# Kernel tuning notes

Measured on AMD Instinct MI355X. Metric: run time of the kernel, lower is better.

## Reference

```python
import jax, jax.numpy as jnp
import numpy as np

NS_STEPS = 10
NS_A, NS_B, NS_C = 3.4445, -4.7750, 2.0315  # standard quintic Newton-Schulz coefficients
EPS = 1e-7

def orthogonalize(w):
    """Newton-Schulz iteration producing a (near-)orthogonal matrix from w."""
    din, dout = w.shape
    transpose = din > dout  # iterate on the wide orientation so X @ X.T is small
    x = w.T if transpose else w
    x = x / (jnp.linalg.norm(x) + EPS)  # spectral norm <= frobenius norm -> contraction

    def body(x, _):
        a = x @ x.T                      # (m, m) Gram matrix
        bmat = NS_B * a + NS_C * (a @ a)
        x = NS_A * x + bmat @ x
        return x, None

    x, _ = jax.lax.scan(body, x, None, length=NS_STEPS)
    return x.T if transpose else x


def setup_inputs() -> dict:
    key = jax.random.key(0)
    k1, k2, k3 = jax.random.split(key, 3)
    B, DIN, DOUT = 16384, 2048, 2048
    x = jax.random.normal(k1, (B, DIN), dtype=jnp.float32)
    w = jax.random.normal(k2, (DIN, DOUT), dtype=jnp.float32)
    b = jax.random.normal(k3, (DOUT,), dtype=jnp.float32) * 0.02
    return {"x": x, "w": w, "b": b}


def reference(x, w, b):
    w_orth = orthogonalize(w)
    return x @ w_orth + b
```

## Files before the change

### kernel.cpp

```cpp
#include <hip/hip_runtime.h>
#include <stdint.h>

typedef unsigned short u16;
typedef _Float16 half_t;
typedef __attribute__((ext_vector_type(4))) float f32x4;
typedef __attribute__((ext_vector_type(8))) _Float16 f16x8;

#define NS_A 3.4445f
#define NS_B -4.7750f
#define NS_C 2.0315f

#define SX      64.0f
#define INV_SX  (1.0f / 64.0f)
#define INV_SA  (1.0f / 4096.0f)

typedef const __attribute__((address_space(1))) void* as1_cvp;
typedef __attribute__((address_space(3))) void* as3_vp;
#define GLOAD_LDS16(gp, lp) \
    __builtin_amdgcn_global_load_lds((as1_cvp)(const void*)(gp), (as3_vp)(void*)(lp), 16, 0, 0)

template <int N> __device__ __forceinline__ void vmwait() {
    if constexpr (N == 0)      asm volatile("s_waitcnt vmcnt(0)" ::: "memory");
    else if constexpr (N == 4) asm volatile("s_waitcnt vmcnt(4)" ::: "memory");
    else if constexpr (N == 6) asm volatile("s_waitcnt vmcnt(6)" ::: "memory");
    else if constexpr (N == 8) asm volatile("s_waitcnt vmcnt(8)" ::: "memory");
    else static_assert(N == 0, "unsupported vmcnt");
}

template <int MODE>
__global__ __launch_bounds__(256, 2) void gemm_ns(
    const half_t* __restrict__ A, const half_t* __restrict__ B,
    const half_t* __restrict__ aux,
    void* __restrict__ outp, half_t* __restrict__ outpT,
    int M, int N, int K)
{
    __shared__ half_t As[3][64 * 64];
    __shared__ half_t Bs[3][128 * 64];
    const int tid  = threadIdx.x;
    const int wid  = tid >> 6;
    const int lane = tid & 63;
    const int wr = wid >> 1, wc = wid & 1;

    int bid = blockIdx.x;
    const int cpx = gridDim.x >> 3;
    bid = (bid & 7) * cpx + (bid >> 3);
    const int nbx  = N / 128;
    const int brow = (bid / nbx) * 64;
    const int bcol = (bid % nbx) * 128;

    f32x4 acc[2][4] = {};

    const int r0   = tid >> 3;
    const int csrc = ((tid & 7) ^ ((tid >> 3) & 7)) * 8;
    const half_t* gA = A + (size_t)(brow + r0) * K + csrc;
    const half_t* gB = B + (size_t)(bcol + r0) * K + csrc;

    auto stage = [&](int slot, int kt) {
#pragma unroll
        for (int j = 0; j < 2; ++j)
            GLOAD_LDS16(gA + (size_t)(j * 32) * K + kt, &As[slot][(j * 256 + wid * 64) * 8]);
#pragma unroll
        for (int j = 0; j < 4; ++j)
            GLOAD_LDS16(gB + (size_t)(j * 32) * K + kt, &Bs[slot][(j * 256 + wid * 64) * 8]);
    };

    f16x8 af[2][2], bf[4][2];
    auto reads = [&](int slot) {
#pragma unroll
        for (int m = 0; m < 2; ++m) {
            const int row = wr * 32 + m * 16 + (lane & 15);
#pragma unroll
            for (int kk = 0; kk < 2; ++kk) {
                const int cc = (kk * 4 + (lane >> 4)) ^ (row & 7);
                af[m][kk] = *(const f16x8*)&As[slot][row * 64 + cc * 8];
            }
        }
#pragma unroll
        for (int n = 0; n < 4; ++n) {
            const int row = wc * 64 + n * 16 + (lane & 15);
#pragma unroll
            for (int kk = 0; kk < 2; ++kk) {
                const int cc = (kk * 4 + (lane >> 4)) ^ (row & 7);
                bf[n][kk] = *(const f16x8*)&Bs[slot][row * 64 + cc * 8];
            }
        }
    };
    auto mfma = [&]() {
        __builtin_amdgcn_s_setprio(1);
#pragma unroll
        for (int kk = 0; kk < 2; ++kk)
#pragma unroll
            for (int m = 0; m < 2; ++m)
#pragma unroll
                for (int n = 0; n < 4; ++n)
                    acc[m][n] = __builtin_amdgcn_mfma_f32_16x16x32_f16(af[m][kk], bf[n][kk], acc[m][n], 0, 0, 0);
        __builtin_amdgcn_s_setprio(0);
    };

    const int nsteps = K / 64;
    stage(0, 0);
    stage(1, 64);
    vmwait<6>();
    __builtin_amdgcn_s_barrier();

    int s = 0;
    for (; s < nsteps - 2; ++s) {
        reads(s % 3);
        stage((s + 2) % 3, (s + 2) * 64);
        vmwait<6>();
        __builtin_amdgcn_s_barrier();
        mfma();
        __builtin_amdgcn_s_barrier();
    }
    reads(s % 3);
    vmwait<0>();
    __builtin_amdgcn_s_barrier();
    mfma();
    __builtin_amdgcn_s_barrier();
    ++s;
    reads(s % 3);
    mfma();

#pragma unroll
    for (int m = 0; m < 2; ++m) {
#pragma unroll
        for (int n = 0; n < 4; ++n) {
            const int row0 = brow + wr * 32 + m * 16 + (lane >> 4) * 4;
            const int col  = bcol + wc * 64 + n * 16 + (lane & 15);
#pragma unroll
            for (int r = 0; r < 4; ++r) {
                const size_t idx = (size_t)(row0 + r) * N + col;
                const float v = acc[m][n][r];
                if (MODE == 0) {
                    ((half_t*)outp)[idx] = (half_t)v;
                } else if (MODE == 1) {
                    ((half_t*)outp)[idx] = (half_t)(NS_B * (float)aux[idx] + NS_C * v * INV_SA);
                } else {
                    const half_t o = (half_t)(NS_A * (float)aux[idx] + v * INV_SA);
                    ((half_t*)outp)[idx] = o;
                    if (outpT) outpT[(size_t)col * M + row0 + r] = o;
                }
            }
        }
    }
}

__global__ __launch_bounds__(512, 2) void gemm_fin(
    const half_t* __restrict__ A, const half_t* __restrict__ B,
    const float* __restrict__ bias, float* __restrict__ out,
    int M, int N, int K)
{
    __shared__ half_t As[4][256 * 32];
    __shared__ half_t Bs[4][256 * 32];
    const int tid  = threadIdx.x;
    const int wid  = tid >> 6;
    const int lane = tid & 63;
    const int wm = wid >> 2;
    const int wn = wid & 3;

    int bid = blockIdx.x;
    const int cpx = gridDim.x >> 3;
    bid = (bid & 7) * cpx + (bid >> 3);
    const int nbx  = N >> 8;
    const int brow = (bid / nbx) << 8;
    const int bcol = (bid % nbx) << 8;

    f32x4 acc[8][4] = {};

    const int r0   = tid >> 2;
    const int csrc = ((tid & 3) ^ ((tid >> 3) & 3)) * 8;
    const half_t* gA = A + (size_t)(brow + r0) * K + csrc;
    const half_t* gB = B + (size_t)(bcol + r0) * K + csrc;

    auto stage = [&](int slot, int kt) {
#pragma unroll
        for (int j = 0; j < 2; ++j)
            GLOAD_LDS16(gA + (size_t)(j * 128) * K + kt, &As[slot][(j * 512 + wid * 64) * 8]);
#pragma unroll
        for (int j = 0; j < 2; ++j)
            GLOAD_LDS16(gB + (size_t)(j * 128) * K + kt, &Bs[slot][(j * 512 + wid * 64) * 8]);
    };

    f16x8 bf[4], af[4];
    auto reads_pre = [&](int slot) {
#pragma unroll
        for (int fc = 0; fc < 4; ++fc) {
            const int row = wn * 64 + fc * 16 + (lane & 15);
            bf[fc] = *(const f16x8*)&Bs[slot][row * 32 + (((lane >> 4) ^ ((row >> 1) & 3)) * 8)];
        }
#pragma unroll
        for (int fr = 0; fr < 4; ++fr) {
            const int row = wm * 128 + fr * 16 + (lane & 15);
            af[fr] = *(const f16x8*)&As[slot][row * 32 + (((lane >> 4) ^ ((row >> 1) & 3)) * 8)];
        }
    };
    auto mfma_all = [&](int slot) {
        __builtin_amdgcn_s_setprio(1);
#pragma unroll
        for (int fr = 0; fr < 4; ++fr)
#pragma unroll
            for (int fc = 0; fc < 4; ++fc)
                acc[fr][fc] = __builtin_amdgcn_mfma_f32_16x16x32_f16(af[fr], bf[fc], acc[fr][fc], 0, 0, 0);
#pragma unroll
        for (int fr = 0; fr < 4; ++fr) {
            const int row = wm * 128 + (fr + 4) * 16 + (lane & 15);
            af[fr] = *(const f16x8*)&As[slot][row * 32 + (((lane >> 4) ^ ((row >> 1) & 3)) * 8)];
        }
#pragma unroll
        for (int fr = 0; fr < 4; ++fr)
#pragma unroll
            for (int fc = 0; fc < 4; ++fc)
                acc[fr + 4][fc] = __builtin_amdgcn_mfma_f32_16x16x32_f16(af[fr], bf[fc], acc[fr + 4][fc], 0, 0, 0);
        __builtin_amdgcn_s_setprio(0);
    };

    const int nsteps = K >> 5;
    stage(0, 0);
    stage(1, 32);
    stage(2, 64);
    vmwait<8>();
    __builtin_amdgcn_s_barrier();

    int s = 0;
    for (; s < nsteps - 3; ++s) {
        reads_pre(s & 3);
        stage((s + 3) & 3, (s + 3) * 32);
        vmwait<8>();
        __builtin_amdgcn_s_barrier();
        mfma_all(s & 3);
        __builtin_amdgcn_s_barrier();
    }
    reads_pre(s & 3);
    vmwait<4>();
    __builtin_amdgcn_s_barrier();
    mfma_all(s & 3);
    __builtin_amdgcn_s_barrier();
    ++s;
    reads_pre(s & 3);
    vmwait<0>();
    __builtin_amdgcn_s_barrier();
    mfma_all(s & 3);
    __builtin_amdgcn_s_barrier();
    ++s;
    reads_pre(s & 3);
    mfma_all(s & 3);

#pragma unroll
    for (int fr = 0; fr < 8; ++fr) {
#pragma unroll
        for (int fc = 0; fc < 4; ++fc) {
            const int row0 = brow + wm * 128 + fr * 16 + (lane >> 4) * 4;
            const int col  = bcol + wn * 64 + fc * 16 + (lane & 15);
            const float bv = bias[col];
#pragma unroll
            for (int r = 0; r < 4; ++r)
                out[(size_t)(row0 + r) * N + col] = acc[fr][fc][r] * INV_SX + bv;
        }
    }
}

__global__ __launch_bounds__(256) void k_sumsq(const float* __restrict__ w,
                                               float* __restrict__ part, int n) {
    __shared__ float s[256];
    const int per  = n / 1024;
    const int base = blockIdx.x * per;
    float acc = 0.f;
    for (int i = threadIdx.x; i < per; i += 256) {
        float v = w[base + i];
        acc += v * v;
    }
    s[threadIdx.x] = acc;
    __syncthreads();
    for (int k = 128; k > 0; k >>= 1) {
        if (threadIdx.x < k) s[threadIdx.x] += s[threadIdx.x + k];
        __syncthreads();
    }
    if (threadIdx.x == 0) part[blockIdx.x] = s[0];
}

__global__ __launch_bounds__(256) void k_scalefin(const float* __restrict__ part,
                                                  float* __restrict__ scale) {
    __shared__ float s[256];
    float acc = 0.f;
    for (int i = threadIdx.x; i < 1024; i += 256) acc += part[i];
    s[threadIdx.x] = acc;
    __syncthreads();
    for (int k = 128; k > 0; k >>= 1) {
        if (threadIdx.x < k) s[threadIdx.x] += s[threadIdx.x + k];
        __syncthreads();
    }
    if (threadIdx.x == 0) scale[0] = SX / (sqrtf(s[0]) + 1e-7f);
}

__global__ __launch_bounds__(256) void k_scale_f16(const float* __restrict__ w,
                                                   const float* __restrict__ scale,
                                                   half_t* __restrict__ o, int n) {
    const int i = (blockIdx.x * 256 + threadIdx.x) * 4;
    if (i < n) {
        const float sc = scale[0];
        float4 v = *(const float4*)(w + i);
        o[i + 0] = (half_t)(v.x * sc);
        o[i + 1] = (half_t)(v.y * sc);
        o[i + 2] = (half_t)(v.z * sc);
        o[i + 3] = (half_t)(v.w * sc);
    }
}

__global__ __launch_bounds__(256) void k_cast_f16(const float* __restrict__ w,
                                                  half_t* __restrict__ o, int n) {
    const int i = (blockIdx.x * 256 + threadIdx.x) * 4;
    if (i < n) {
        float4 v = *(const float4*)(w + i);
        o[i + 0] = (half_t)v.x;
        o[i + 1] = (half_t)v.y;
        o[i + 2] = (half_t)v.z;
        o[i + 3] = (half_t)v.w;
    }
}

__global__ __launch_bounds__(256) void k_transpose(const u16* __restrict__ in,
                                                   u16* __restrict__ out, int n) {
    __shared__ u16 tile[64][65];
    const int bx = blockIdx.x * 64, by = blockIdx.y * 64;
    const int tx = threadIdx.x & 63, ty = threadIdx.x >> 6;
    for (int i = ty; i < 64; i += 4) tile[i][tx] = in[(size_t)(by + i) * n + bx + tx];
    __syncthreads();
    for (int i = ty; i < 64; i += 4) out[(size_t)(bx + i) * n + by + tx] = tile[tx][i];
}

extern "C" void kernel_launch(void* const* d_in, const int* in_sizes, int n_in,
                              void* d_out, int out_size, void* d_ws, size_t ws_size,
                              hipStream_t stream) {
    const float* x = (const float*)d_in[0];
    const float* w = (const float*)d_in[1];
    const float* b = (const float*)d_in[2];
    float* out = (float*)d_out;

    const int D  = 2048;
    const int Bm = in_sizes[0] / D;
    const int WN = D * D;
    const int XN = Bm * D;

    const size_t matB = (size_t)WN * 2;
    const bool pingpong = ws_size >= 8192 + 6 * matB + (size_t)XN * 2;

    char* ws = (char*)d_ws;
    float* part  = (float*)ws;
    float* scale = part + 1024;
    half_t* xb0  = (half_t*)(ws + 8192);
    half_t* xb1  = xb0 + WN;
    half_t* xbTa = xb1 + WN;
    half_t* xbTb = pingpong ? (xbTa + WN) : xbTa;
    half_t* amat = xbTb + WN;
    half_t* bmat = amat + WN;
    half_t* xinb = bmat + WN;

    k_sumsq<<<1024, 256, 0, stream>>>(w, part, WN);
    k_scalefin<<<1, 256, 0, stream>>>(part, scale);
    k_scale_f16<<<WN / 4 / 256, 256, 0, stream>>>(w, scale, xb0, WN);

    k_cast_f16<<<XN / 4 / 256, 256, 0, stream>>>(x, xinb, XN);

    const dim3 tgrid(D / 64, D / 64);
    k_transpose<<<tgrid, 256, 0, stream>>>((const u16*)xb0, (u16*)xbTa, D);

    const int ns_grid = (D / 64) * (D / 128);

    half_t* cur = xb0;
    half_t* nxt = xb1;
    half_t* Tr  = xbTa;
    half_t* Tw  = xbTb;
    for (int it = 0; it < 10; ++it) {
        gemm_ns<0><<<ns_grid, 256, 0, stream>>>(cur, cur, nullptr, amat, nullptr, D, D, D);
        gemm_ns<1><<<ns_grid, 256, 0, stream>>>(amat, amat, amat, bmat, nullptr, D, D, D);
        if (pingpong) {
            gemm_ns<2><<<ns_grid, 256, 0, stream>>>(bmat, Tr, cur, nxt, Tw, D, D, D);
            half_t* tt = Tr; Tr = Tw; Tw = tt;
        } else {
            gemm_ns<2><<<ns_grid, 256, 0, stream>>>(bmat, Tr, cur, nxt, nullptr, D, D, D);
            k_transpose<<<tgrid, 256, 0, stream>>>((const u16*)nxt, (u16*)Tr, D);
        }
        half_t* t = cur; cur = nxt; nxt = t;
    }

    const int fin_grid = (Bm / 256) * (D / 256);
    gemm_fin<<<fin_grid, 512, 0, stream>>>(xinb, Tr, b, out, Bm, D, D);
}
```

Measured before the change: 982.1 us.

## Use 2-wave Newton-Schulz GEMM blocks and unroll final GEMM pipeline by four

```diff
diff --git a/kernel.cpp b/kernel.cpp
--- a/kernel.cpp
+++ b/kernel.cpp
@@ -20,15 +20,15 @@
     __builtin_amdgcn_global_load_lds((as1_cvp)(const void*)(gp), (as3_vp)(void*)(lp), 16, 0, 0)
 
 template <int N> __device__ __forceinline__ void vmwait() {
-    if constexpr (N == 0)      asm volatile("s_waitcnt vmcnt(0)" ::: "memory");
-    else if constexpr (N == 4) asm volatile("s_waitcnt vmcnt(4)" ::: "memory");
-    else if constexpr (N == 6) asm volatile("s_waitcnt vmcnt(6)" ::: "memory");
-    else if constexpr (N == 8) asm volatile("s_waitcnt vmcnt(8)" ::: "memory");
+    if constexpr (N == 0)       asm volatile("s_waitcnt vmcnt(0)" ::: "memory");
+    else if constexpr (N == 4)  asm volatile("s_waitcnt vmcnt(4)" ::: "memory");
+    else if constexpr (N == 8)  asm volatile("s_waitcnt vmcnt(8)" ::: "memory");
+    else if constexpr (N == 12) asm volatile("s_waitcnt vmcnt(12)" ::: "memory");
     else static_assert(N == 0, "unsupported vmcnt");
 }
 
 template <int MODE>
-__global__ __launch_bounds__(256, 2) void gemm_ns(
+__global__ __launch_bounds__(128) void gemm_ns(
     const half_t* __restrict__ A, const half_t* __restrict__ B,
     const half_t* __restrict__ aux,
     void* __restrict__ outp, half_t* __restrict__ outpT,
@@ -39,7 +39,6 @@
     const int tid  = threadIdx.x;
     const int wid  = tid >> 6;
     const int lane = tid & 63;
-    const int wr = wid >> 1, wc = wid & 1;
 
     int bid = blockIdx.x;
     const int cpx = gridDim.x >> 3;
@@ -48,7 +47,7 @@
     const int brow = (bid / nbx) * 64;
     const int bcol = (bid % nbx) * 128;
 
-    f32x4 acc[2][4] = {};
+    f32x4 acc[4][4] = {};
 
     const int r0   = tid >> 3;
     const int csrc = ((tid & 7) ^ ((tid >> 3) & 7)) * 8;
@@ -57,18 +56,18 @@
 
     auto stage = [&](int slot, int kt) {
 #pragma unroll
-        for (int j = 0; j < 2; ++j)
-            GLOAD_LDS16(gA + (size_t)(j * 32) * K + kt, &As[slot][(j * 256 + wid * 64) * 8]);
-#pragma unroll
         for (int j = 0; j < 4; ++j)
-            GLOAD_LDS16(gB + (size_t)(j * 32) * K + kt, &Bs[slot][(j * 256 + wid * 64) * 8]);
-    };
-
-    f16x8 af[2][2], bf[4][2];
+            GLOAD_LDS16(gA + (size_t)(j * 16) * K + kt, &As[slot][(j * 128 + wid * 64) * 8]);
+#pragma unroll
+        for (int j = 0; j < 8; ++j)
+            GLOAD_LDS16(gB + (size_t)(j * 16) * K + kt, &Bs[slot][(j * 128 + wid * 64) * 8]);
+    };
+
+    f16x8 af[4][2], bf[4][2];
     auto reads = [&](int slot) {
 #pragma unroll
-        for (int m = 0; m < 2; ++m) {
-            const int row = wr * 32 + m * 16 + (lane & 15);
+        for (int m = 0; m < 4; ++m) {
+            const int row = m * 16 + (lane & 15);
 #pragma unroll
             for (int kk = 0; kk < 2; ++kk) {
                 const int cc = (kk * 4 + (lane >> 4)) ^ (row & 7);
@@ -77,7 +76,7 @@
         }
 #pragma unroll
         for (int n = 0; n < 4; ++n) {
-            const int row = wc * 64 + n * 16 + (lane & 15);
+            const int row = wid * 64 + n * 16 + (lane & 15);
 #pragma unroll
             for (int kk = 0; kk < 2; ++kk) {
                 const int cc = (kk * 4 + (lane >> 4)) ^ (row & 7);
@@ -90,7 +89,7 @@
 #pragma unroll
         for (int kk = 0; kk < 2; ++kk)
 #pragma unroll
-            for (int m = 0; m < 2; ++m)
+            for (int m = 0; m < 4; ++m)
 #pragma unroll
                 for (int n = 0; n < 4; ++n)
                     acc[m][n] = __builtin_amdgcn_mfma_f32_16x16x32_f16(af[m][kk], bf[n][kk], acc[m][n], 0, 0, 0);
@@ -100,14 +99,14 @@
     const int nsteps = K / 64;
     stage(0, 0);
     stage(1, 64);
-    vmwait<6>();
+    vmwait<12>();
     __builtin_amdgcn_s_barrier();
 
     int s = 0;
     for (; s < nsteps - 2; ++s) {
         reads(s % 3);
         stage((s + 2) % 3, (s + 2) * 64);
-        vmwait<6>();
+        vmwait<12>();
         __builtin_amdgcn_s_barrier();
         mfma();
         __builtin_amdgcn_s_barrier();
@@ -122,11 +121,11 @@
     mfma();
 
 #pragma unroll
-    for (int m = 0; m < 2; ++m) {
+    for (int m = 0; m < 4; ++m) {
 #pragma unroll
         for (int n = 0; n < 4; ++n) {
-            const int row0 = brow + wr * 32 + m * 16 + (lane >> 4) * 4;
-            const int col  = bcol + wc * 64 + n * 16 + (lane & 15);
+            const int row0 = brow + m * 16 + (lane >> 4) * 4;
+            const int col  = bcol + wid * 64 + n * 16 + (lane & 15);
 #pragma unroll
             for (int r = 0; r < 4; ++r) {
                 const size_t idx = (size_t)(row0 + r) * N + col;
@@ -180,70 +179,53 @@
         for (int j = 0; j < 2; ++j)
             GLOAD_LDS16(gB + (size_t)(j * 128) * K + kt, &Bs[slot][(j * 512 + wid * 64) * 8]);
     };
-
-    f16x8 bf[4], af[4];
-    auto reads_pre = [&](int slot) {
+    auto compute = [&](int slot) {
+        f16x8 af[8], bf[4];
+#pragma unroll
+        for (int fr = 0; fr < 8; ++fr) {
+            const int row = wm * 128 + fr * 16 + (lane & 15);
+            af[fr] = *(const f16x8*)&As[slot][row * 32 + (((lane >> 4) ^ ((row >> 1) & 3)) * 8)];
+        }
 #pragma unroll
         for (int fc = 0; fc < 4; ++fc) {
             const int row = wn * 64 + fc * 16 + (lane & 15);
             bf[fc] = *(const f16x8*)&Bs[slot][row * 32 + (((lane >> 4) ^ ((row >> 1) & 3)) * 8)];
         }
-#pragma unroll
-        for (int fr = 0; fr < 4; ++fr) {
-            const int row = wm * 128 + fr * 16 + (lane & 15);
-            af[fr] = *(const f16x8*)&As[slot][row * 32 + (((lane >> 4) ^ ((row >> 1) & 3)) * 8)];
-        }
-    };
-    auto mfma_all = [&](int slot) {
         __builtin_amdgcn_s_setprio(1);
 #pragma unroll
-        for (int fr = 0; fr < 4; ++fr)
+        for (int fr = 0; fr < 8; ++fr)
 #pragma unroll
             for (int fc = 0; fc < 4; ++fc)
                 acc[fr][fc] = __builtin_amdgcn_mfma_f32_16x16x32_f16(af[fr], bf[fc], acc[fr][fc], 0, 0, 0);
-#pragma unroll
-        for (int fr = 0; fr < 4; ++fr) {
-            const int row = wm * 128 + (fr + 4) * 16 + (lane & 15);
-            af[fr] = *(const f16x8*)&As[slot][row * 32 + (((lane >> 4) ^ ((row >> 1) & 3)) * 8)];
-        }
-#pragma unroll
-        for (int fr = 0; fr < 4; ++fr)
-#pragma unroll
-            for (int fc = 0; fc < 4; ++fc)
-                acc[fr + 4][fc] = __builtin_amdgcn_mfma_f32_16x16x32_f16(af[fr], bf[fc], acc[fr + 4][fc], 0, 0, 0);
         __builtin_amdgcn_s_setprio(0);
     };
 
-    const int nsteps = K >> 5;
     stage(0, 0);
     stage(1, 32);
     stage(2, 64);
-    vmwait<8>();
-    __builtin_amdgcn_s_barrier();
-
-    int s = 0;
-    for (; s < nsteps - 3; ++s) {
-        reads_pre(s & 3);
-        stage((s + 3) & 3, (s + 3) * 32);
-        vmwait<8>();
-        __builtin_amdgcn_s_barrier();
-        mfma_all(s & 3);
-        __builtin_amdgcn_s_barrier();
-    }
-    reads_pre(s & 3);
-    vmwait<4>();
-    __builtin_amdgcn_s_barrier();
-    mfma_all(s & 3);
-    __builtin_amdgcn_s_barrier();
-    ++s;
-    reads_pre(s & 3);
-    vmwait<0>();
-    __builtin_amdgcn_s_barrier();
-    mfma_all(s & 3);
-    __builtin_amdgcn_s_barrier();
-    ++s;
-    reads_pre(s & 3);
-    mfma_all(s & 3);
+    int kt_next = 96;
+
+#define RSTEP(SLOT, DOSTAGE, VMN) \
+    do { \
+        if (DOSTAGE) { stage((SLOT + 3) & 3, kt_next); kt_next += 32; } \
+        vmwait<VMN>(); \
+        __builtin_amdgcn_s_barrier(); \
+        compute(SLOT); \
+        __builtin_amdgcn_s_barrier(); \
+    } while (0)
+
+    const int nouter = ((K >> 5) - 4) >> 2;
+    for (int tt = 0; tt < nouter; ++tt) {
+        RSTEP(0, true, 12);
+        RSTEP(1, true, 12);
+        RSTEP(2, true, 12);
+        RSTEP(3, true, 12);
+    }
+    RSTEP(0, true, 12);
+    RSTEP(1, false, 8);
+    RSTEP(2, false, 4);
+    RSTEP(3, false, 0);
+#undef RSTEP
 
 #pragma unroll
     for (int fr = 0; fr < 8; ++fr) {
@@ -371,13 +353,13 @@
     half_t* Tr  = xbTa;
     half_t* Tw  = xbTb;
     for (int it = 0; it < 10; ++it) {
-        gemm_ns<0><<<ns_grid, 256, 0, stream>>>(cur, cur, nullptr, amat, nullptr, D, D, D);
-        gemm_ns<1><<<ns_grid, 256, 0, stream>>>(amat, amat, amat, bmat, nullptr, D, D, D);
+        gemm_ns<0><<<ns_grid, 128, 0, stream>>>(cur, cur, nullptr, amat, nullptr, D, D, D);
+        gemm_ns<1><<<ns_grid, 128, 0, stream>>>(amat, amat, amat, bmat, nullptr, D, D, D);
         if (pingpong) {
-            gemm_ns<2><<<ns_grid, 256, 0, stream>>>(bmat, Tr, cur, nxt, Tw, D, D, D);
+            gemm_ns<2><<<ns_grid, 128, 0, stream>>>(bmat, Tr, cur, nxt, Tw, D, D, D);
             half_t* tt = Tr; Tr = Tw; Tw = tt;
         } else {
-            gemm_ns<2><<<ns_grid, 256, 0, stream>>>(bmat, Tr, cur, nxt, nullptr, D, D, D);
+            gemm_ns<2><<<ns_grid, 128, 0, stream>>>(bmat, Tr, cur, nxt, nullptr, D, D, D);
             k_transpose<<<tgrid, 256, 0, stream>>>((const u16*)nxt, (u16*)Tr, D);
         }
         half_t* t = cur; cur = nxt; nxt = t;
```

New measurement: 1.087 ms. 10.7% more time.

## Interleave A/B staging with half-tile MFMA phases and remap NS GEMM blocks

Applied to the files above, without the earlier changes.

```diff
diff --git a/kernel.cpp b/kernel.cpp
--- a/kernel.cpp
+++ b/kernel.cpp
@@ -20,10 +20,11 @@
     __builtin_amdgcn_global_load_lds((as1_cvp)(const void*)(gp), (as3_vp)(void*)(lp), 16, 0, 0)
 
 template <int N> __device__ __forceinline__ void vmwait() {
-    if constexpr (N == 0)      asm volatile("s_waitcnt vmcnt(0)" ::: "memory");
-    else if constexpr (N == 4) asm volatile("s_waitcnt vmcnt(4)" ::: "memory");
-    else if constexpr (N == 6) asm volatile("s_waitcnt vmcnt(6)" ::: "memory");
-    else if constexpr (N == 8) asm volatile("s_waitcnt vmcnt(8)" ::: "memory");
+    if constexpr (N == 0)       asm volatile("s_waitcnt vmcnt(0)" ::: "memory");
+    else if constexpr (N == 4)  asm volatile("s_waitcnt vmcnt(4)" ::: "memory");
+    else if constexpr (N == 6)  asm volatile("s_waitcnt vmcnt(6)" ::: "memory");
+    else if constexpr (N == 8)  asm volatile("s_waitcnt vmcnt(8)" ::: "memory");
+    else if constexpr (N == 12) asm volatile("s_waitcnt vmcnt(12)" ::: "memory");
     else static_assert(N == 0, "unsupported vmcnt");
 }
 
@@ -41,12 +42,10 @@
     const int lane = tid & 63;
     const int wr = wid >> 1, wc = wid & 1;
 
-    int bid = blockIdx.x;
-    const int cpx = gridDim.x >> 3;
-    bid = (bid & 7) * cpx + (bid >> 3);
-    const int nbx  = N / 128;
-    const int brow = (bid / nbx) * 64;
-    const int bcol = (bid % nbx) * 128;
+    const int xcd = blockIdx.x & 7;
+    const int ii  = blockIdx.x >> 3;
+    const int brow = ((xcd & 1) * 16 + (ii >> 2)) * 64;
+    const int bcol = ((xcd >> 1) * 4 + (ii & 3)) * 128;
 
     f32x4 acc[2][4] = {};
 
@@ -172,78 +171,93 @@
     const half_t* gA = A + (size_t)(brow + r0) * K + csrc;
     const half_t* gB = B + (size_t)(bcol + r0) * K + csrc;
 
-    auto stage = [&](int slot, int kt) {
+    auto stage_a = [&](int slot, int kt) {
 #pragma unroll
         for (int j = 0; j < 2; ++j)
             GLOAD_LDS16(gA + (size_t)(j * 128) * K + kt, &As[slot][(j * 512 + wid * 64) * 8]);
+    };
+    auto stage_b = [&](int slot, int kt) {
 #pragma unroll
         for (int j = 0; j < 2; ++j)
             GLOAD_LDS16(gB + (size_t)(j * 128) * K + kt, &Bs[slot][(j * 512 + wid * 64) * 8]);
     };
 
     f16x8 bf[4], af[4];
-    auto reads_pre = [&](int slot) {
+    auto read_b = [&](int slot) {
 #pragma unroll
         for (int fc = 0; fc < 4; ++fc) {
             const int row = wn * 64 + fc * 16 + (lane & 15);
             bf[fc] = *(const f16x8*)&Bs[slot][row * 32 + (((lane >> 4) ^ ((row >> 1) & 3)) * 8)];
         }
+    };
+    auto read_a = [&](int slot, int base) {
 #pragma unroll
         for (int fr = 0; fr < 4; ++fr) {
-            const int row = wm * 128 + fr * 16 + (lane & 15);
+            const int row = wm * 128 + (base + fr) * 16 + (lane & 15);
             af[fr] = *(const f16x8*)&As[slot][row * 32 + (((lane >> 4) ^ ((row >> 1) & 3)) * 8)];
         }
     };
-    auto mfma_all = [&](int slot) {
+    auto mfma_half = [&](int base) {
         __builtin_amdgcn_s_setprio(1);
 #pragma unroll
         for (int fr = 0; fr < 4; ++fr)
 #pragma unroll
             for (int fc = 0; fc < 4; ++fc)
-                acc[fr][fc] = __builtin_amdgcn_mfma_f32_16x16x32_f16(af[fr], bf[fc], acc[fr][fc], 0, 0, 0);
-#pragma unroll
-        for (int fr = 0; fr < 4; ++fr) {
-            const int row = wm * 128 + (fr + 4) * 16 + (lane & 15);
-            af[fr] = *(const f16x8*)&As[slot][row * 32 + (((lane >> 4) ^ ((row >> 1) & 3)) * 8)];
-        }
-#pragma unroll
-        for (int fr = 0; fr < 4; ++fr)
-#pragma unroll
-            for (int fc = 0; fc < 4; ++fc)
-                acc[fr + 4][fc] = __builtin_amdgcn_mfma_f32_16x16x32_f16(af[fr], bf[fc], acc[fr + 4][fc], 0, 0, 0);
+                acc[base + fr][fc] = __builtin_amdgcn_mfma_f32_16x16x32_f16(af[fr], bf[fc], acc[base + fr][fc], 0, 0, 0);
         __builtin_amdgcn_s_setprio(0);
     };
 
     const int nsteps = K >> 5;
-    stage(0, 0);
-    stage(1, 32);
-    stage(2, 64);
+    stage_a(0, 0);  stage_b(0, 0);
+    stage_a(1, 32); stage_b(1, 32);
+    stage_a(2, 64); stage_b(2, 64);
     vmwait<8>();
     __builtin_amdgcn_s_barrier();
 
     int s = 0;
     for (; s < nsteps - 3; ++s) {
-        reads_pre(s & 3);
-        stage((s + 3) & 3, (s + 3) * 32);
-        vmwait<8>();
-        __builtin_amdgcn_s_barrier();
-        mfma_all(s & 3);
-        __builtin_amdgcn_s_barrier();
-    }
-    reads_pre(s & 3);
-    vmwait<4>();
-    __builtin_amdgcn_s_barrier();
-    mfma_all(s & 3);
-    __builtin_amdgcn_s_barrier();
-    ++s;
-    reads_pre(s & 3);
-    vmwait<0>();
-    __builtin_amdgcn_s_barrier();
-    mfma_all(s & 3);
-    __builtin_amdgcn_s_barrier();
-    ++s;
-    reads_pre(s & 3);
-    mfma_all(s & 3);
+        const int slot = s & 3;
+        const int kt3  = (s + 3) * 32;
+        read_b(slot);
+        read_a(slot, 0);
+        stage_a((s + 3) & 3, kt3);
+        vmwait<6>();
+        __builtin_amdgcn_s_barrier();
+        mfma_half(0);
+        read_a(slot, 4);
+        stage_b((s + 3) & 3, kt3);
+        __builtin_amdgcn_s_barrier();
+        mfma_half(4);
+    }
+    {
+        const int slot = s & 3;
+        read_b(slot); read_a(slot, 0);
+        vmwait<4>();
+        __builtin_amdgcn_s_barrier();
+        mfma_half(0);
+        read_a(slot, 4);
+        __builtin_amdgcn_s_barrier();
+        mfma_half(4);
+        ++s;
+    }
+    {
+        const int slot = s & 3;
+        read_b(slot); read_a(slot, 0);
+        vmwait<0>();
+        __builtin_amdgcn_s_barrier();
+        mfma_half(0);
+        read_a(slot, 4);
+        __builtin_amdgcn_s_barrier();
+        mfma_half(4);
+        ++s;
+    }
+    {
+        const int slot = s & 3;
+        read_b(slot); read_a(slot, 0);
+        mfma_half(0);
+        read_a(slot, 4);
+        mfma_half(4);
+    }
 
 #pragma unroll
     for (int fr = 0; fr < 8; ++fr) {
```

Result: faster. 952.8 us (-3.0%).
